# Kernel optimization log

Measured on AMD Instinct MI355X. Metric: run time of the kernel, lower is better.

## Reference

```python
import jax, jax.numpy as jnp
import numpy as np

N_NODES = 100000
N_EDGES = 1600000
N_GRAPHS = 256
D = 128
L = 3
N_OUT = 10


def setup_inputs() -> dict:
    key = jax.random.key(0)
    ks = jax.random.split(key, 6)
    x = jax.random.normal(ks[0], (N_NODES, D), dtype=jnp.float32)
    edge_index = jax.random.randint(ks[1], (2, N_EDGES), 0, N_NODES, dtype=jnp.int64)
    batch = jnp.sort(jax.random.randint(ks[2], (N_NODES,), 0, N_GRAPHS, dtype=jnp.int64))
    conv_w = jax.random.normal(ks[3], (L, D, D), dtype=jnp.float32) * (1.0 / np.sqrt(D))
    conv_b = jnp.zeros((L, D), dtype=jnp.float32)
    out_w = jax.random.normal(ks[4], (3 * D, N_OUT), dtype=jnp.float32) * (1.0 / np.sqrt(3 * D))
    out_b = jnp.zeros((N_OUT,), dtype=jnp.float32)
    return {"x": x, "edge_index": edge_index, "batch": batch,
            "conv_w": conv_w, "conv_b": conv_b, "out_w": out_w, "out_b": out_b}


def reference(x, edge_index, batch, conv_w, conv_b, out_w, out_b):
    N = x.shape[0]
    # --- add self-loops (PyG GCNConv default) ---
    loop = jnp.arange(N, dtype=edge_index.dtype)
    src = jnp.concatenate([edge_index[0], loop])  # [E+N]
    dst = jnp.concatenate([edge_index[1], loop])
    # --- symmetric normalization: deg computed on dst (col) ---
    deg = jax.ops.segment_sum(jnp.ones_like(dst, dtype=x.dtype), dst, num_segments=N)
    dinv = jnp.where(deg > 0, jax.lax.rsqrt(jnp.maximum(deg, 1.0)), 0.0)
    norm = dinv[src] * dinv[dst]  # [E+N]

    h = x
    for l in range(conv_w.shape[0]):
        h = h @ conv_w[l]                                   # [N, D] transform first
        msg = h[src] * norm[:, None]                        # gather + scale
        h = jax.ops.segment_sum(msg, dst, num_segments=N)   # scatter-add
        h = jax.nn.relu(h + conv_b[l])

    # --- global max / mean / add pooling over graphs ---
    B = N_GRAPHS
    gmax = jax.ops.segment_max(h, batch, num_segments=B)
    gsum = jax.ops.segment_sum(h, batch, num_segments=B)
    cnt = jax.ops.segment_sum(jnp.ones((N, 1), h.dtype), batch, num_segments=B)
    gmean = gsum / jnp.maximum(cnt, 1.0)
    pooled = jnp.concatenate([gmax, gmean, gsum], axis=1)   # [B, 3D]
    # dropout p=0.5 is identity in eval mode
    return pooled @ out_w + out_b
```

## Files before the change

kernel.cpp:

```cpp
#include <hip/hip_runtime.h>
#include <hip/hip_bf16.h>

#define D 128
#define NP 8
#define DPB 64
#define KPB (DPB * NP)
#define SUB 64
#define CAP_SUB 64

typedef __attribute__((ext_vector_type(8))) __bf16 bf16x8;
typedef __attribute__((ext_vector_type(4))) float f32x4;
typedef __attribute__((ext_vector_type(4))) short s16x4;
typedef __attribute__((ext_vector_type(8))) short s16x8;

static __device__ __forceinline__ short f2bf(float f) {
    union { float f; unsigned u; } in; in.f = f;
    unsigned u = in.u;
    u += 0x7fffu + ((u >> 16) & 1u);
    return (short)(u >> 16);
}

__global__ void k_bucket(const int* __restrict__ src, const int* __restrict__ dst,
                         int* __restrict__ bcnt, int* __restrict__ staging,
                         int E, int KBE) {
    int i = blockIdx.x * 256 + threadIdx.x;
    if (i >= E) return;
    int d = dst[i], s = src[i];
    int b = d >> 6;
    int key = ((d & 63) << 3) | (s >> 14);
    int j = blockIdx.x & (SUB - 1);
    int slot = atomicAdd(&bcnt[j * KBE + b], 1);
    if (slot < CAP_SUB) staging[((size_t)j * KBE + b) * CAP_SUB + slot] = (key << 17) | s;
}

__global__ void k_bscan(const int* __restrict__ bcnt, int* __restrict__ bbase,
                        int* __restrict__ row_ptr, int nkeys, int KBE) {
    __shared__ int sm[512];
    __shared__ int carry;
    int t = threadIdx.x;
    if (t == 0) carry = 0;
    __syncthreads();
    for (int c0 = 0; c0 < KBE; c0 += 512) {
        int b = c0 + t;
        int v = 0;
        if (b < KBE) {
            for (int j = 0; j < SUB; j++) {
                int c = bcnt[j * KBE + b];
                v += (c > CAP_SUB) ? CAP_SUB : c;
            }
        }
        sm[t] = v;
        __syncthreads();
        for (int off = 1; off < 512; off <<= 1) {
            int x = (t >= off) ? sm[t - off] : 0;
            __syncthreads();
            sm[t] += x;
            __syncthreads();
        }
        if (b < KBE) bbase[b] = sm[t] - v + carry;
        __syncthreads();
        if (t == 0) carry += sm[511];
        __syncthreads();
    }
    if (t == 0) row_ptr[nkeys] = carry;
}

__global__ __launch_bounds__(256) void k_build(
    const int* __restrict__ staging, const int* __restrict__ bcnt,
    const int* __restrict__ bbase, int* __restrict__ row_ptr,
    int* __restrict__ csr_src, float* __restrict__ dinv, int N, int KBE)
{
    const int b = blockIdx.x;
    const int tid = threadIdx.x;
    __shared__ int cnt[KPB];
    __shared__ int suboff[SUB + 1];
    __shared__ int chunkbuf[256];
    __shared__ int carry;

    if (tid < SUB) {
        int c = bcnt[tid * KBE + b];
        suboff[tid + 1] = (c > CAP_SUB) ? CAP_SUB : c;
    }
    for (int k = tid; k < KPB; k += 256) cnt[k] = 0;
    if (tid == 0) { suboff[0] = 0; carry = 0; }
    __syncthreads();
    if (tid == 0)
        for (int j = 1; j <= SUB; j++) suboff[j] += suboff[j - 1];
    __syncthreads();
    const int nb = suboff[SUB];
    const int base = bbase[b];

    for (int t = tid; t < nb; t += 256) {
        int lo = 0, hi = SUB;
        while (lo + 1 < hi) { int mid = (lo + hi) >> 1; if (suboff[mid] <= t) lo = mid; else hi = mid; }
        int w = staging[((size_t)lo * KBE + b) * CAP_SUB + (t - suboff[lo])];
        atomicAdd(&cnt[w >> 17], 1);
    }
    __syncthreads();

    #pragma unroll 1
    for (int c = 0; c < KPB / 256; c++) {
        int idx = c * 256 + tid;
        int v = cnt[idx];
        chunkbuf[tid] = v;
        __syncthreads();
        for (int off = 1; off < 256; off <<= 1) {
            int x = (tid >= off) ? chunkbuf[tid - off] : 0;
            __syncthreads();
            chunkbuf[tid] += x;
            __syncthreads();
        }
        cnt[idx] = chunkbuf[tid] - v + carry;
        __syncthreads();
        if (tid == 255) carry += chunkbuf[255];
        __syncthreads();
    }

    for (int k = tid; k < KPB; k += 256)
        row_ptr[(size_t)b * KPB + k] = base + cnt[k];
    for (int dl = tid; dl < DPB; dl += 256) {
        int d = b * DPB + dl;
        if (d < N) {
            int hi2 = (dl == DPB - 1) ? nb : cnt[(dl + 1) * NP];
            int deg = hi2 - cnt[dl * NP];
            dinv[d] = rsqrtf((float)deg + 1.0f);
        }
    }
    __syncthreads();

    for (int t = tid; t < nb; t += 256) {
        int lo = 0, hi = SUB;
        while (lo + 1 < hi) { int mid = (lo + hi) >> 1; if (suboff[mid] <= t) lo = mid; else hi = mid; }
        int w = staging[((size_t)lo * KBE + b) * CAP_SUB + (t - suboff[lo])];
        int slot = base + atomicAdd(&cnt[w >> 17], 1);
        csr_src[slot] = w & 0x1FFFF;
    }
}

__global__ void k_gseg(const int* __restrict__ batch, int* __restrict__ gstart,
                       int* __restrict__ gcnt, int N, int B) {
    int g = blockIdx.x * blockDim.x + threadIdx.x;
    if (g > B) return;
    int lo = 0, hi = N;
    while (lo < hi) {
        int mid = (lo + hi) >> 1;
        if (batch[mid] < g) lo = mid + 1; else hi = mid;
    }
    gstart[g] = lo;
    if (g < B) {
        int lo2 = lo, hi2 = N;
        while (lo2 < hi2) {
            int mid = (lo2 + hi2) >> 1;
            if (batch[mid] < g + 1) lo2 = mid + 1; else hi2 = mid;
        }
        gcnt[g] = lo2 - lo;
    }
}

__global__ void k_cvt_x(const float* __restrict__ x, const float* __restrict__ dinv,
                        short* __restrict__ xb, int total4) {
    int i = blockIdx.x * blockDim.x + threadIdx.x;
    if (i < total4) {
        float d = dinv[i >> 5];
        float4 v = ((const float4*)x)[i];
        s16x4 o;
        o.x = f2bf(v.x * d); o.y = f2bf(v.y * d);
        o.z = f2bf(v.z * d); o.w = f2bf(v.w * d);
        ((s16x4*)xb)[i] = o;
    }
}

__global__ void k_cvt_w(const float* __restrict__ W, short* __restrict__ Wt, int total) {
    int i = blockIdx.x * blockDim.x + threadIdx.x;
    if (i < total) {
        int l = i >> 14;
        int rem = i & 16383;
        int n = rem >> 7;
        int k = rem & 127;
        Wt[i] = f2bf(W[(l << 14) + (k << 7) + n]);
    }
}

__global__ __launch_bounds__(256) void k_layer(
    const short* __restrict__ hin, const int* __restrict__ row_ptr,
    const int* __restrict__ csr_src, const float* __restrict__ dinv,
    const short* __restrict__ Wt, const float* __restrict__ bias,
    short* __restrict__ hout, float* __restrict__ hrelu, int N, int mode)
{
    __shared__ __align__(16) short tile[16 * 128];
    const int tid = threadIdx.x;
    const int wave = tid >> 6;
    const int lane = tid & 63;
    const int group = lane >> 4;
    const int lg = lane & 15;
    const int off = lg * 8;
    const int node_base = blockIdx.x * 16;
    const int r = wave * 4 + group;
    const int i = node_base + r;

    short* dstp = &tile[r * 128 + ((lg ^ (r & 7)) << 3)];
    if (i < N) {
        float acc[8];
        bf16x8 v = *(const bf16x8*)(hin + (size_t)i * D + off);
        #pragma unroll
        for (int k = 0; k < 8; k++) acc[k] = (float)v[k];
        const int kb = i * NP;
        int s = row_ptr[kb];
        #pragma unroll 1
        for (int p = 0; p < NP; p++) {
            int e = row_ptr[kb + p + 1];
            for (int t = s; t < e; t += 4) {
                int i0 = csr_src[t];
                int i1 = (t + 1 < e) ? csr_src[t + 1] : -1;
                int i2 = (t + 2 < e) ? csr_src[t + 2] : -1;
                int i3 = (t + 3 < e) ? csr_src[t + 3] : -1;
                bf16x8 v0 = *(const bf16x8*)(hin + (size_t)i0 * D + off);
                bf16x8 v1, v2, v3;
                if (i1 >= 0) v1 = *(const bf16x8*)(hin + (size_t)i1 * D + off);
                if (i2 >= 0) v2 = *(const bf16x8*)(hin + (size_t)i2 * D + off);
                if (i3 >= 0) v3 = *(const bf16x8*)(hin + (size_t)i3 * D + off);
                #pragma unroll
                for (int k = 0; k < 8; k++) acc[k] += (float)v0[k];
                if (i1 >= 0) {
                    #pragma unroll
                    for (int k = 0; k < 8; k++) acc[k] += (float)v1[k];
                }
                if (i2 >= 0) {
                    #pragma unroll
                    for (int k = 0; k < 8; k++) acc[k] += (float)v2[k];
                }
                if (i3 >= 0) {
                    #pragma unroll
                    for (int k = 0; k < 8; k++) acc[k] += (float)v3[k];
                }
            }
            s = e;
        }
        const float di = dinv[i];
        s16x8 o;
        #pragma unroll
        for (int k = 0; k < 8; k++) o[k] = f2bf(acc[k] * di);
        *(s16x8*)dstp = o;
    } else {
        s16x8 z = {0, 0, 0, 0, 0, 0, 0, 0};
        *(s16x8*)dstp = z;
    }
    __syncthreads();

    bf16x8 afrag[4];
    #pragma unroll
    for (int kt = 0; kt < 4; kt++)
        afrag[kt] = *(const bf16x8*)(&tile[lg * 128 + (((group + 4 * kt) ^ (lg & 7)) << 3)]);

    f32x4 acc2[2];
    #pragma unroll
    for (int nt = 0; nt < 2; nt++) { f32x4 z = {0.f, 0.f, 0.f, 0.f}; acc2[nt] = z; }
    #pragma unroll
    for (int nt = 0; nt < 2; nt++) {
        const short* bp = Wt + (size_t)(wave * 32 + nt * 16 + lg) * D + group * 8;
        #pragma unroll
        for (int kt = 0; kt < 4; kt++) {
            bf16x8 b = *(const bf16x8*)(bp + kt * 32);
            acc2[nt] = __builtin_amdgcn_mfma_f32_16x16x32_bf16(afrag[kt], b, acc2[nt], 0, 0, 0);
        }
    }

    float bcol[2];
    #pragma unroll
    for (int nt = 0; nt < 2; nt++) bcol[nt] = bias[wave * 32 + nt * 16 + lg];
    const int row0 = node_base + group * 4;
    #pragma unroll
    for (int i2 = 0; i2 < 4; i2++) {
        int r2 = row0 + i2;
        if (r2 < N) {
            if (mode == 0) {
                float dr = dinv[r2];
                #pragma unroll
                for (int nt = 0; nt < 2; nt++) {
                    int col = wave * 32 + nt * 16 + lg;
                    float val = fmaxf(acc2[nt][i2] + bcol[nt], 0.0f);
                    hout[(size_t)r2 * D + col] = f2bf(val * dr);
                }
            } else {
                #pragma unroll
                for (int nt = 0; nt < 2; nt++) {
                    int col = wave * 32 + nt * 16 + lg;
                    hrelu[(size_t)r2 * D + col] = fmaxf(acc2[nt][i2] + bcol[nt], 0.0f);
                }
            }
        }
    }
}

__global__ __launch_bounds__(256) void k_pool(const float* __restrict__ hrelu,
                                              const int* __restrict__ gstart,
                                              const int* __restrict__ gcnt,
                                              float* __restrict__ gmax,
                                              float* __restrict__ gsum) {
    int g = blockIdx.x;
    int c = threadIdx.x & 127;
    int p = threadIdx.x >> 7;
    int start = gstart[g];
    int endr = start + gcnt[g];

    float mx0 = 0.f, mx1 = 0.f, sm0 = 0.f, sm1 = 0.f;
    int r = start + p;
    for (; r + 2 < endr; r += 4) {
        float v0 = hrelu[(size_t)r * D + c];
        float v1 = hrelu[(size_t)(r + 2) * D + c];
        mx0 = fmaxf(mx0, v0); sm0 += v0;
        mx1 = fmaxf(mx1, v1); sm1 += v1;
    }
    if (r < endr) {
        float v0 = hrelu[(size_t)r * D + c];
        mx0 = fmaxf(mx0, v0); sm0 += v0;
    }
    float mx = fmaxf(mx0, mx1), sm = sm0 + sm1;

    __shared__ float smx[128], ssm[128];
    if (p == 1) { smx[c] = mx; ssm[c] = sm; }
    __syncthreads();
    if (p == 0) {
        gmax[g * D + c] = fmaxf(mx, smx[c]);
        gsum[g * D + c] = sm + ssm[c];
    }
}

__global__ void k_final(const float* __restrict__ gmax, const float* __restrict__ gsum,
                        const int* __restrict__ gcnt, const float* __restrict__ ow,
                        const float* __restrict__ ob, float* __restrict__ out) {
    int g = blockIdx.x;
    int t = threadIdx.x;
    float part[10];
    #pragma unroll
    for (int o = 0; o < 10; o++) part[o] = 0.f;
    float invc = 1.0f / fmaxf((float)gcnt[g], 1.0f);
    for (int k = t; k < 3 * D; k += 64) {
        float pk;
        if (k < D) pk = gmax[g * D + k];
        else if (k < 2 * D) pk = gsum[g * D + (k - D)] * invc;
        else pk = gsum[g * D + (k - 2 * D)];
        const float* w = ow + k * 10;
        #pragma unroll
        for (int o = 0; o < 10; o++) part[o] += pk * w[o];
    }
    #pragma unroll
    for (int off = 32; off > 0; off >>= 1)
        #pragma unroll
        for (int o = 0; o < 10; o++) part[o] += __shfl_down(part[o], off, 64);
    if (t == 0)
        #pragma unroll
        for (int o = 0; o < 10; o++) out[g * 10 + o] = part[o] + ob[o];
}

extern "C" void kernel_launch(void* const* d_in, const int* in_sizes, int n_in,
                              void* d_out, int out_size, void* d_ws, size_t ws_size,
                              hipStream_t stream) {
    const float* x     = (const float*)d_in[0];
    const int*   ei    = (const int*)d_in[1];
    const int*   batch = (const int*)d_in[2];
    const float* convw = (const float*)d_in[3];
    const float* convb = (const float*)d_in[4];
    const float* outw  = (const float*)d_in[5];
    const float* outb  = (const float*)d_in[6];
    float* out = (float*)d_out;

    const int N = in_sizes[0] / D;
    const int E = in_sizes[1] / 2;
    const int L = in_sizes[3] / (D * D);
    const int B = out_size / 10;

    const int* src = ei;
    const int* dst = ei + E;

    const int KBE   = (N + DPB - 1) / DPB;
    const int nkeys = KBE * KPB;

    char* p = (char*)d_ws;
    auto alloc = [&](size_t bytes) { char* r = p; p += (bytes + 255) & ~255ull; return r; };
    short* hb0     = (short*)alloc((size_t)N * D * 2);
    short* hb1     = (short*)alloc((size_t)N * D * 2);
    float* hrelu   = (float*)alloc((size_t)N * D * 4);
    short* Wt      = (short*)alloc((size_t)L * D * D * 2);
    int*   row_ptr = (int*)alloc(((size_t)nkeys + 1) * 4);
    int*   csr_src = (int*)alloc((size_t)E * 4);
    int*   bcnt    = (int*)alloc((size_t)SUB * KBE * 4);
    int*   bbase   = (int*)alloc((size_t)KBE * 4);
    float* dinv    = (float*)alloc((size_t)N * 4);
    float* gmax    = (float*)alloc((size_t)B * D * 4);
    float* gsum    = (float*)alloc((size_t)B * D * 4);
    int*   gcnt    = (int*)alloc((size_t)B * 4);
    int*   gstart  = (int*)alloc(((size_t)B + 1) * 4);

    int* staging = (int*)hrelu;

    hipMemsetAsync(bcnt, 0, (size_t)SUB * KBE * 4, stream);

    k_bucket<<<(E + 255) / 256, 256, 0, stream>>>(src, dst, bcnt, staging, E, KBE);
    k_gseg<<<1, 512, 0, stream>>>(batch, gstart, gcnt, N, B);
    k_bscan<<<1, 512, 0, stream>>>(bcnt, bbase, row_ptr, nkeys, KBE);
    k_build<<<KBE, 256, 0, stream>>>(staging, bcnt, bbase, row_ptr, csr_src, dinv, N, KBE);
    k_cvt_x<<<((N * D / 4) + 255) / 256, 256, 0, stream>>>(x, dinv, hb0, N * D / 4);
    k_cvt_w<<<((L * D * D) + 255) / 256, 256, 0, stream>>>(convw, Wt, L * D * D);

    const int lblocks = (N + 15) / 16;
    k_layer<<<lblocks, 256, 0, stream>>>(hb0, row_ptr, csr_src, dinv, Wt,
                                         convb, hb1, hrelu, N, 0);
    k_layer<<<lblocks, 256, 0, stream>>>(hb1, row_ptr, csr_src, dinv, Wt + D * D,
                                         convb + D, hb0, hrelu, N, 0);
    k_layer<<<lblocks, 256, 0, stream>>>(hb0, row_ptr, csr_src, dinv, Wt + 2 * D * D,
                                         convb + 2 * D, hb1, hrelu, N, 1);

    k_pool<<<B, 256, 0, stream>>>(hrelu, gstart, gcnt, gmax, gsum);
    k_final<<<B, 64, 0, stream>>>(gmax, gsum, gcnt, outw, outb, out);
}
```

Baseline: 494.9 us.

## Parallelize bucket totals, drop binary search in build, split pooling across blocks

Moves the per-bucket sum of sub-bucket counts out of the single-block scan into a separate parallel kernel, so the one-block scan only prefix-sums totals. k_build now assigns four threads per sub-bucket and walks its staging region directly instead of binary-searching a prefix of sub-bucket offsets, and takes its edge count from consecutive bbase entries. Pooling is split into four blocks per graph that write partial max and sum, which k_final then reduces. This adds one kernel launch and a partial-buffer reduction in exchange for more parallelism in the serial preprocessing and pooling stages.

```diff
diff --git a/kernel.cpp b/kernel.cpp
--- a/kernel.cpp
+++ b/kernel.cpp
@@ -33,7 +33,19 @@
     if (slot < CAP_SUB) staging[((size_t)j * KBE + b) * CAP_SUB + slot] = (key << 17) | s;
 }
 
-__global__ void k_bscan(const int* __restrict__ bcnt, int* __restrict__ bbase,
+__global__ void k_btot(const int* __restrict__ bcnt, int* __restrict__ btot, int KBE) {
+    int b = blockIdx.x * 256 + threadIdx.x;
+    if (b >= KBE) return;
+    int v = 0;
+    #pragma unroll
+    for (int j = 0; j < SUB; j++) {
+        int c = bcnt[j * KBE + b];
+        v += (c > CAP_SUB) ? CAP_SUB : c;
+    }
+    btot[b] = v;
+}
+
+__global__ void k_bscan(const int* __restrict__ btot, int* __restrict__ bbase,
                         int* __restrict__ row_ptr, int nkeys, int KBE) {
     __shared__ int sm[512];
     __shared__ int carry;
@@ -42,13 +54,7 @@
     __syncthreads();
     for (int c0 = 0; c0 < KBE; c0 += 512) {
         int b = c0 + t;
-        int v = 0;
-        if (b < KBE) {
-            for (int j = 0; j < SUB; j++) {
-                int c = bcnt[j * KBE + b];
-                v += (c > CAP_SUB) ? CAP_SUB : c;
-            }
-        }
+        int v = (b < KBE) ? btot[b] : 0;
         sm[t] = v;
         __syncthreads();
         for (int off = 1; off < 512; off <<= 1) {
@@ -62,7 +68,7 @@
         if (t == 0) carry += sm[511];
         __syncthreads();
     }
-    if (t == 0) row_ptr[nkeys] = carry;
+    if (t == 0) { bbase[KBE] = carry; row_ptr[nkeys] = carry; }
 }
 
 __global__ __launch_bounds__(256) void k_build(
@@ -73,29 +79,26 @@
     const int b = blockIdx.x;
     const int tid = threadIdx.x;
     __shared__ int cnt[KPB];
-    __shared__ int suboff[SUB + 1];
+    __shared__ int subn[SUB];
     __shared__ int chunkbuf[256];
     __shared__ int carry;
 
     if (tid < SUB) {
         int c = bcnt[tid * KBE + b];
-        suboff[tid + 1] = (c > CAP_SUB) ? CAP_SUB : c;
+        subn[tid] = (c > CAP_SUB) ? CAP_SUB : c;
     }
     for (int k = tid; k < KPB; k += 256) cnt[k] = 0;
-    if (tid == 0) { suboff[0] = 0; carry = 0; }
-    __syncthreads();
-    if (tid == 0)
-        for (int j = 1; j <= SUB; j++) suboff[j] += suboff[j - 1];
-    __syncthreads();
-    const int nb = suboff[SUB];
+    if (tid == 0) carry = 0;
+    __syncthreads();
+
     const int base = bbase[b];
-
-    for (int t = tid; t < nb; t += 256) {
-        int lo = 0, hi = SUB;
-        while (lo + 1 < hi) { int mid = (lo + hi) >> 1; if (suboff[mid] <= t) lo = mid; else hi = mid; }
-        int w = staging[((size_t)lo * KBE + b) * CAP_SUB + (t - suboff[lo])];
-        atomicAdd(&cnt[w >> 17], 1);
-    }
+    const int nb = bbase[b + 1] - base;
+    const int j = tid >> 2, l4 = tid & 3;
+    const int* __restrict__ sreg = staging + ((size_t)j * KBE + b) * CAP_SUB;
+    const int sn = subn[j];
+
+    for (int e = l4; e < sn; e += 4)
+        atomicAdd(&cnt[sreg[e] >> 17], 1);
     __syncthreads();
 
     #pragma unroll 1
@@ -128,10 +131,8 @@
     }
     __syncthreads();
 
-    for (int t = tid; t < nb; t += 256) {
-        int lo = 0, hi = SUB;
-        while (lo + 1 < hi) { int mid = (lo + hi) >> 1; if (suboff[mid] <= t) lo = mid; else hi = mid; }
-        int w = staging[((size_t)lo * KBE + b) * CAP_SUB + (t - suboff[lo])];
+    for (int e = l4; e < sn; e += 4) {
+        int w = sreg[e];
         int slot = base + atomicAdd(&cnt[w >> 17], 1);
         csr_src[slot] = w & 0x1FFFF;
     }
@@ -295,19 +296,20 @@
 __global__ __launch_bounds__(256) void k_pool(const float* __restrict__ hrelu,
                                               const int* __restrict__ gstart,
                                               const int* __restrict__ gcnt,
-                                              float* __restrict__ gmax,
-                                              float* __restrict__ gsum) {
-    int g = blockIdx.x;
+                                              float* __restrict__ pmax,
+                                              float* __restrict__ psum, int B) {
+    int g = blockIdx.x >> 2;
+    int q = blockIdx.x & 3;
     int c = threadIdx.x & 127;
     int p = threadIdx.x >> 7;
     int start = gstart[g];
     int endr = start + gcnt[g];
 
     float mx0 = 0.f, mx1 = 0.f, sm0 = 0.f, sm1 = 0.f;
-    int r = start + p;
-    for (; r + 2 < endr; r += 4) {
+    int r = start + q * 2 + p;
+    for (; r + 8 < endr; r += 16) {
         float v0 = hrelu[(size_t)r * D + c];
-        float v1 = hrelu[(size_t)(r + 2) * D + c];
+        float v1 = hrelu[(size_t)(r + 8) * D + c];
         mx0 = fmaxf(mx0, v0); sm0 += v0;
         mx1 = fmaxf(mx1, v1); sm1 += v1;
     }
@@ -321,14 +323,14 @@
     if (p == 1) { smx[c] = mx; ssm[c] = sm; }
     __syncthreads();
     if (p == 0) {
-        gmax[g * D + c] = fmaxf(mx, smx[c]);
-        gsum[g * D + c] = sm + ssm[c];
-    }
-}
-
-__global__ void k_final(const float* __restrict__ gmax, const float* __restrict__ gsum,
+        pmax[((size_t)q * B + g) * D + c] = fmaxf(mx, smx[c]);
+        psum[((size_t)q * B + g) * D + c] = sm + ssm[c];
+    }
+}
+
+__global__ void k_final(const float* __restrict__ pmax, const float* __restrict__ psum,
                         const int* __restrict__ gcnt, const float* __restrict__ ow,
-                        const float* __restrict__ ob, float* __restrict__ out) {
+                        const float* __restrict__ ob, float* __restrict__ out, int B) {
     int g = blockIdx.x;
     int t = threadIdx.x;
     float part[10];
@@ -336,10 +338,19 @@
     for (int o = 0; o < 10; o++) part[o] = 0.f;
     float invc = 1.0f / fmaxf((float)gcnt[g], 1.0f);
     for (int k = t; k < 3 * D; k += 64) {
+        int c = (k < D) ? k : ((k < 2 * D) ? k - D : k - 2 * D);
         float pk;
-        if (k < D) pk = gmax[g * D + k];
-        else if (k < 2 * D) pk = gsum[g * D + (k - D)] * invc;
-        else pk = gsum[g * D + (k - 2 * D)];
+        if (k < D) {
+            float m = pmax[(size_t)g * D + c];
+            #pragma unroll
+            for (int q = 1; q < 4; q++) m = fmaxf(m, pmax[((size_t)q * B + g) * D + c]);
+            pk = m;
+        } else {
+            float s = psum[(size_t)g * D + c];
+            #pragma unroll
+            for (int q = 1; q < 4; q++) s += psum[((size_t)q * B + g) * D + c];
+            pk = (k < 2 * D) ? s * invc : s;
+        }
         const float* w = ow + k * 10;
         #pragma unroll
         for (int o = 0; o < 10; o++) part[o] += pk * w[o];
@@ -385,10 +396,11 @@
     int*   row_ptr = (int*)alloc(((size_t)nkeys + 1) * 4);
     int*   csr_src = (int*)alloc((size_t)E * 4);
     int*   bcnt    = (int*)alloc((size_t)SUB * KBE * 4);
-    int*   bbase   = (int*)alloc((size_t)KBE * 4);
+    int*   btot    = (int*)alloc((size_t)KBE * 4);
+    int*   bbase   = (int*)alloc(((size_t)KBE + 1) * 4);
     float* dinv    = (float*)alloc((size_t)N * 4);
-    float* gmax    = (float*)alloc((size_t)B * D * 4);
-    float* gsum    = (float*)alloc((size_t)B * D * 4);
+    float* pmax    = (float*)alloc((size_t)4 * B * D * 4);
+    float* psum    = (float*)alloc((size_t)4 * B * D * 4);
     int*   gcnt    = (int*)alloc((size_t)B * 4);
     int*   gstart  = (int*)alloc(((size_t)B + 1) * 4);
 
@@ -398,7 +410,8 @@
 
     k_bucket<<<(E + 255) / 256, 256, 0, stream>>>(src, dst, bcnt, staging, E, KBE);
     k_gseg<<<1, 512, 0, stream>>>(batch, gstart, gcnt, N, B);
-    k_bscan<<<1, 512, 0, stream>>>(bcnt, bbase, row_ptr, nkeys, KBE);
+    k_btot<<<(KBE + 255) / 256, 256, 0, stream>>>(bcnt, btot, KBE);
+    k_bscan<<<1, 512, 0, stream>>>(btot, bbase, row_ptr, nkeys, KBE);
     k_build<<<KBE, 256, 0, stream>>>(staging, bcnt, bbase, row_ptr, csr_src, dinv, N, KBE);
     k_cvt_x<<<((N * D / 4) + 255) / 256, 256, 0, stream>>>(x, dinv, hb0, N * D / 4);
     k_cvt_w<<<((L * D * D) + 255) / 256, 256, 0, stream>>>(convw, Wt, L * D * D);
@@ -411,6 +424,6 @@
     k_layer<<<lblocks, 256, 0, stream>>>(hb0, row_ptr, csr_src, dinv, Wt + 2 * D * D,
                                          convb + 2 * D, hb1, hrelu, N, 1);
 
-    k_pool<<<B, 256, 0, stream>>>(hrelu, gstart, gcnt, gmax, gsum);
-    k_final<<<B, 64, 0, stream>>>(gmax, gsum, gcnt, outw, outb, out);
-}
+    k_pool<<<B * 4, 256, 0, stream>>>(hrelu, gstart, gcnt, pmax, psum, B);
+    k_final<<<B, 64, 0, stream>>>(pmax, psum, gcnt, outw, outb, out, B);
+}
```

Result: faster. 469.6 us (-5.1%).
